# Kernel tuning notes

Measured on AMD Instinct MI355X. Metric: run time of the kernel, lower is better.

Reference implementation:

```python
import jax, jax.numpy as jnp
import numpy as np

H = 16          # num_heads
K = 15          # kernel_size (padding_l = K-1, causal)
EPS = 1e-5      # LayerNorm eps


def setup_inputs() -> dict:
    key = jax.random.key(0)
    ks = jax.random.split(key, 8)
    T, B, C, F = 1024, 8, 1024, 4096
    n = lambda k, shape, scale=1.0: jax.random.normal(k, shape, jnp.float32) * scale
    return {
        "x": n(ks[0], (T, B, C)),
        "w_lin": n(ks[1], (C, H * K), 0.02),      # dynamic-conv weight projection
        "b_lin": jnp.zeros((H * K,), jnp.float32),
        "ln_g": jnp.ones((C,), jnp.float32),
        "ln_b": jnp.zeros((C,), jnp.float32),
        "fc1_w": n(ks[2], (C, F), 0.02),
        "fc1_b": jnp.zeros((F,), jnp.float32),
        "fc2_w": n(ks[3], (F, C), 0.02),
        "fc2_b": jnp.zeros((C,), jnp.float32),
    }


def _dynamic_conv(x, w_lin, b_lin):
    # x: (T, B, C). Per-timestep weights -> softmax over kernel -> causal conv.
    T, B, C = x.shape
    R = C // H  # channels per head
    w = jnp.einsum('tbc,ck->tbk', x, w_lin) + b_lin          # (T, B, H*K)
    w = jax.nn.softmax(w.reshape(T, B, H, K), axis=-1)        # softmax over kernel taps
    # causal left-padding: tap k sees x[t + k - (K-1)]
    xp = jnp.pad(x, ((K - 1, 0), (0, 0), (0, 0))).reshape(T + K - 1, B, H, R)
    o = jnp.zeros((T, B, H, R), x.dtype)
    for k in range(K):  # fixed small kernel loop; avoids (T,B,C,K) unfold tensor
        o = o + w[:, :, :, k:k + 1] * xp[k:k + T]
    return o.reshape(T, B, C)


def _layer_norm(y, g, b):
    mu = jnp.mean(y, axis=-1, keepdims=True)
    var = jnp.var(y, axis=-1, keepdims=True)
    return (y - mu) * jax.lax.rsqrt(var + EPS) * g + b


def _forward(x, w_lin, b_lin, ln_g, ln_b, fc1_w, fc1_b, fc2_w, fc2_b):
    y = _dynamic_conv(x, w_lin, b_lin)
    y = _layer_norm(y, ln_g, ln_b)
    h = jax.nn.relu(jnp.einsum('tbc,cf->tbf', y, fc1_w) + fc1_b)
    out = jnp.einsum('tbf,fc->tbc', h, fc2_w) + fc2_b
    return out + y  # residual around FFN (residual taken post-LayerNorm)


def reference(x, w_lin, b_lin, ln_g, ln_b, fc1_w, fc1_b, fc2_w, fc2_b):
    return _forward(x, w_lin, b_lin, ln_g, ln_b, fc1_w, fc1_b, fc2_w, fc2_b)
```

## Files before the change

kernel.cpp:

```cpp
#include <hip/hip_runtime.h>


#define T_DIM 1024
#define B_DIM 8
#define C_DIM 1024
#define F_DIM 4096
#define H_DIM 16
#define K_TAP 15
#define TB (T_DIM * B_DIM)

typedef __attribute__((ext_vector_type(8))) short short8;
typedef __attribute__((ext_vector_type(4))) float f32x4;

__device__ __forceinline__ float bf2f(unsigned short u) {
    union { unsigned int i; float f; } v; v.i = ((unsigned int)u) << 16; return v.f;
}
__device__ __forceinline__ unsigned short f2bf(float f) {
    union { float f; unsigned int i; } v; v.f = f;
    unsigned int r = v.i + 0x7fffu + ((v.i >> 16) & 1u);
    return (unsigned short)(r >> 16);
}

__device__ __forceinline__ void async_copy16(const void* gptr, void* lptr) {
    __builtin_amdgcn_global_load_lds(
        (const __attribute__((address_space(1))) void*)gptr,
        (__attribute__((address_space(3))) void*)lptr, 16, 0, 0);
}

__global__ __launch_bounds__(256)
void prep(const float* __restrict__ x, unsigned short* __restrict__ xb,
          const float* __restrict__ fc1_w, unsigned short* __restrict__ fc1T,
          const float* __restrict__ fc2_w, unsigned short* __restrict__ fc2T,
          const float* __restrict__ w_lin, unsigned short* __restrict__ wlinT) {
    const int bid = blockIdx.x;
    const int tid = threadIdx.x;
    if (bid < 2048) {
        const int idx = bid * 256 + tid;
#pragma unroll
        for (int it = 0; it < 4; it++) {
            int i = (idx + it * 524288) * 4;
            float4 v = *(const float4*)(x + i);
            uint2 o;
            o.x = (unsigned int)f2bf(v.x) | ((unsigned int)f2bf(v.y) << 16);
            o.y = (unsigned int)f2bf(v.z) | ((unsigned int)f2bf(v.w) << 16);
            *(uint2*)(xb + i) = o;
        }
        return;
    }
    const float* in; unsigned short* out; int R, Cin, c0, r0;
    if (bid < 3072) {
        int idx = bid - 2048;
        in = fc1_w; out = fc1T; R = C_DIM; Cin = F_DIM;
        c0 = (idx & 63) * 64; r0 = (idx >> 6) * 64;
    } else if (bid < 4096) {
        int idx = bid - 3072;
        in = fc2_w; out = fc2T; R = F_DIM; Cin = C_DIM;
        c0 = (idx & 15) * 64; r0 = (idx >> 4) * 64;
    } else {
        int idx = bid - 4096;
        in = w_lin; out = wlinT; R = C_DIM; Cin = 240;
        c0 = (idx & 3) * 64; r0 = (idx >> 2) * 64;
    }
    __shared__ unsigned short tile[64][65];
    const int xx = tid & 63, yy = tid >> 6;
#pragma unroll
    for (int j = 0; j < 16; j++) {
        int r = r0 + yy + j * 4, c = c0 + xx;
        unsigned short v = 0;
        if (c < Cin) v = f2bf(in[(size_t)r * Cin + c]);
        tile[yy + j * 4][xx] = v;
    }
    __syncthreads();
#pragma unroll
    for (int j = 0; j < 16; j++) {
        out[(size_t)(c0 + yy + j * 4) * R + (r0 + xx)] = tile[xx][yy + j * 4];
    }
}

template <int MODE, int SWAP>
__global__ __launch_bounds__(256)
void gemm_bt(const unsigned short* __restrict__ A,
             const unsigned short* __restrict__ Bt,
             void* __restrict__ Cout_v,
             int M, int N, int K, int kz,
             const float* __restrict__ bias,
             const unsigned short* __restrict__ resid) {
    __shared__ __align__(16) unsigned short As[2][128 * 64];
    __shared__ __align__(16) unsigned short Bs[2][128 * 64];

    const int tid = threadIdx.x;
    const int m0 = (SWAP ? blockIdx.x : blockIdx.y) * 128;
    const int n0 = (SWAP ? blockIdx.y : blockIdx.x) * 128;
    const int kbase = blockIdx.z * kz;
    const int wave = tid >> 6, lane = tid & 63;
    const int quad = lane >> 4, l16 = lane & 15;
    const int wm = (wave >> 1) * 64;
    const int wn = (wave & 1) * 64;

    f32x4 acc[4][4];
#pragma unroll
    for (int i = 0; i < 4; i++)
#pragma unroll
        for (int j = 0; j < 4; j++) acc[i][j] = (f32x4){0.f, 0.f, 0.f, 0.f};

    const int rsub = lane >> 3;
    const int gch = (lane & 7) ^ rsub;
    const unsigned short* gA = A + (size_t)(m0 + wave * 32 + rsub) * K + kbase + gch * 8;
    const unsigned short* gB = Bt + (size_t)(n0 + wave * 32 + rsub) * K + kbase + gch * 8;
    unsigned short* lA[2] = {&As[0][wave * 32 * 64], &As[1][wave * 32 * 64]};
    unsigned short* lB[2] = {&Bs[0][wave * 32 * 64], &Bs[1][wave * 32 * 64]};

#pragma unroll
    for (int j = 0; j < 4; j++) {
        async_copy16(gA + (size_t)j * 8 * K, lA[0] + j * 8 * 64);
        async_copy16(gB + (size_t)j * 8 * K, lB[0] + j * 8 * 64);
    }

    const int swz = l16 & 7;
    int buf = 0;
    for (int k0 = 0; k0 < kz; k0 += 64) {
        __syncthreads();

        const int nk = k0 + 64;
        if (nk < kz) {
            const int nb = buf ^ 1;
#pragma unroll
            for (int j = 0; j < 4; j++) {
                async_copy16(gA + nk + (size_t)j * 8 * K, lA[nb] + j * 8 * 64);
                async_copy16(gB + nk + (size_t)j * 8 * K, lB[nb] + j * 8 * 64);
            }
        }

        short8 af[2][4], bfr[2][4];
#pragma unroll
        for (int kk = 0; kk < 2; kk++) {
            const int c = kk * 4 + quad;
#pragma unroll
            for (int i = 0; i < 4; i++) {
                af[kk][i]  = *(const short8*)(&As[buf][(wm + i * 16 + l16) * 64 + (c ^ swz) * 8]);
                bfr[kk][i] = *(const short8*)(&Bs[buf][(wn + i * 16 + l16) * 64 + (c ^ swz) * 8]);
            }
        }
#pragma unroll
        for (int kk = 0; kk < 2; kk++)
#pragma unroll
            for (int mi = 0; mi < 4; mi++)
#pragma unroll
                for (int nj = 0; nj < 4; nj++)
                    acc[mi][nj] = __builtin_amdgcn_mfma_f32_16x16x32_bf16(
                        af[kk][mi], bfr[kk][nj], acc[mi][nj], 0, 0, 0);
        buf ^= 1;
    }

    const int crow0 = m0 + wm + quad * 4;
    const int ccol0 = n0 + wn + l16;
    if (MODE == 3) {
        float* Cf = (float*)Cout_v + (size_t)blockIdx.z * M * N;
#pragma unroll
        for (int mi = 0; mi < 4; mi++)
#pragma unroll
            for (int i = 0; i < 4; i++) {
                int rr = crow0 + mi * 16 + i;
#pragma unroll
                for (int nj = 0; nj < 4; nj++)
                    Cf[(size_t)rr * N + ccol0 + nj * 16] = acc[mi][nj][i];
            }
    } else if (MODE == 1) {
        unsigned short* Cb = (unsigned short*)Cout_v;
        float bv[4];
#pragma unroll
        for (int nj = 0; nj < 4; nj++) bv[nj] = bias[ccol0 + nj * 16];
#pragma unroll
        for (int mi = 0; mi < 4; mi++)
#pragma unroll
            for (int i = 0; i < 4; i++) {
                int rr = crow0 + mi * 16 + i;
#pragma unroll
                for (int nj = 0; nj < 4; nj++) {
                    float v = fmaxf(acc[mi][nj][i] + bv[nj], 0.f);
                    Cb[(size_t)rr * N + ccol0 + nj * 16] = f2bf(v);
                }
            }
    } else {
        float* Cf = (float*)Cout_v;
        float bv[4];
#pragma unroll
        for (int nj = 0; nj < 4; nj++) bv[nj] = bias[ccol0 + nj * 16];
#pragma unroll
        for (int mi = 0; mi < 4; mi++)
#pragma unroll
            for (int i = 0; i < 4; i++) {
                int rr = crow0 + mi * 16 + i;
#pragma unroll
                for (int nj = 0; nj < 4; nj++) {
                    float v = acc[mi][nj][i] + bv[nj]
                            + bf2f(resid[(size_t)rr * N + ccol0 + nj * 16]);
                    Cf[(size_t)rr * N + ccol0 + nj * 16] = v;
                }
            }
    }
}

#define XSP 1032
#define WS_STRIDE ((size_t)TB * 256)
__global__ __launch_bounds__(256)
void conv_ln16s(const unsigned short* __restrict__ xb,
                const float* __restrict__ wscore,
                const float* __restrict__ b_lin,
                const float* __restrict__ ln_g,
                const float* __restrict__ ln_b,
                unsigned short* __restrict__ y) {
    __shared__ __align__(16) unsigned short xs[30 * XSP];
    __shared__ float wls[16 * 240];
    const int blk = blockIdx.x;
    const int b = blk & 7;
    const int t0 = (blk >> 3) * 16;
    const int tid = threadIdx.x;
    const int wave = tid >> 6, lane = tid & 63;

    for (int s = wave; s < 60; s += 4) {
        const int row = s >> 1, half = s & 1;
        const int t = t0 + row - 14;
        unsigned short* ldst = &xs[row * XSP + half * 512];
        if (t >= 0) {
            const unsigned short* src =
                xb + ((size_t)t * B_DIM + b) * C_DIM + half * 512 + lane * 8;
            async_copy16(src, ldst);
        } else {
            *(uint4*)(ldst + lane * 8) = make_uint4(0u, 0u, 0u, 0u);
        }
    }

    {
        const int row = tid >> 4, hh = tid & 15;
        const size_t grow = (size_t)(t0 + row) * B_DIM + b;
        const float* p = wscore + grow * 256 + hh * K_TAP;
        float v[K_TAP], mx = -1e30f;
#pragma unroll
        for (int k = 0; k < K_TAP; k++) {
            v[k] = p[k] + p[k + WS_STRIDE] + b_lin[hh * K_TAP + k];
            mx = fmaxf(mx, v[k]);
        }
        float s = 0.f;
#pragma unroll
        for (int k = 0; k < K_TAP; k++) { v[k] = __expf(v[k] - mx); s += v[k]; }
        float inv = 1.0f / s;
#pragma unroll
        for (int k = 0; k < K_TAP; k++) wls[row * 240 + hh * K_TAP + k] = v[k] * inv;
    }
    __syncthreads();

    const int chA = lane * 8;
    const int chB = 512 + lane * 8;
    const int hA = lane >> 3;
    const int hB = 8 + (lane >> 3);
    for (int rj = wave; rj < 16; rj += 4) {
        float o[16];
#pragma unroll
        for (int i = 0; i < 16; i++) o[i] = 0.f;
#pragma unroll
        for (int k = 0; k < K_TAP; k++) {
            float wA = wls[rj * 240 + hA * K_TAP + k];
            float wB = wls[rj * 240 + hB * K_TAP + k];
            const unsigned short* xr = &xs[(rj + k) * XSP];
            uint4 pA = *(const uint4*)(xr + chA);
            uint4 pB = *(const uint4*)(xr + chB);
            unsigned int ua[4] = {pA.x, pA.y, pA.z, pA.w};
            unsigned int ub[4] = {pB.x, pB.y, pB.z, pB.w};
#pragma unroll
            for (int q = 0; q < 4; q++) {
                o[2 * q]     += wA * bf2f((unsigned short)(ua[q] & 0xffff));
                o[2 * q + 1] += wA * bf2f((unsigned short)(ua[q] >> 16));
                o[8 + 2 * q]     += wB * bf2f((unsigned short)(ub[q] & 0xffff));
                o[8 + 2 * q + 1] += wB * bf2f((unsigned short)(ub[q] >> 16));
            }
        }
        float s = 0.f, s2 = 0.f;
#pragma unroll
        for (int i = 0; i < 16; i++) { s += o[i]; s2 += o[i] * o[i]; }
#pragma unroll
        for (int off = 32; off > 0; off >>= 1) {
            s  += __shfl_xor(s, off, 64);
            s2 += __shfl_xor(s2, off, 64);
        }
        float mu = s * (1.0f / C_DIM);
        float var = s2 * (1.0f / C_DIM) - mu * mu;
        float rs = rsqrtf(var + 1e-5f);

        unsigned short o16[16];
#pragma unroll
        for (int i = 0; i < 8; i++)
            o16[i] = f2bf((o[i] - mu) * rs * ln_g[chA + i] + ln_b[chA + i]);
#pragma unroll
        for (int i = 0; i < 8; i++)
            o16[8 + i] = f2bf((o[8 + i] - mu) * rs * ln_g[chB + i] + ln_b[chB + i]);
        uint4 w0, w1;
        w0.x = (unsigned int)o16[0]  | ((unsigned int)o16[1]  << 16);
        w0.y = (unsigned int)o16[2]  | ((unsigned int)o16[3]  << 16);
        w0.z = (unsigned int)o16[4]  | ((unsigned int)o16[5]  << 16);
        w0.w = (unsigned int)o16[6]  | ((unsigned int)o16[7]  << 16);
        w1.x = (unsigned int)o16[8]  | ((unsigned int)o16[9]  << 16);
        w1.y = (unsigned int)o16[10] | ((unsigned int)o16[11] << 16);
        w1.z = (unsigned int)o16[12] | ((unsigned int)o16[13] << 16);
        w1.w = (unsigned int)o16[14] | ((unsigned int)o16[15] << 16);
        unsigned short* yr = y + ((size_t)(t0 + rj) * B_DIM + b) * C_DIM;
        *(uint4*)(yr + chA) = w0;
        *(uint4*)(yr + chB) = w1;
    }
}

extern "C" void kernel_launch(void* const* d_in, const int* in_sizes, int n_in,
                              void* d_out, int out_size, void* d_ws, size_t ws_size,
                              hipStream_t stream) {
    const float* x     = (const float*)d_in[0];
    const float* w_lin = (const float*)d_in[1];
    const float* b_lin = (const float*)d_in[2];
    const float* ln_g  = (const float*)d_in[3];
    const float* ln_b  = (const float*)d_in[4];
    const float* fc1_w = (const float*)d_in[5];
    const float* fc1_b = (const float*)d_in[6];
    const float* fc2_w = (const float*)d_in[7];
    const float* fc2_b = (const float*)d_in[8];
    float* out = (float*)d_out;

    char* ws = (char*)d_ws;
    unsigned short* xb    = (unsigned short*)(ws);
    unsigned short* fc1T  = (unsigned short*)(ws + 16777216);
    unsigned short* fc2T  = (unsigned short*)(ws + 25165824);
    unsigned short* wlinT = (unsigned short*)(ws + 33554432);
    unsigned short* y     = (unsigned short*)(ws + 34078720);
    unsigned short* h     = (unsigned short*)(ws + 50855936);
    float* wscore = (float*)(ws + 50855936);

    prep<<<4160, 256, 0, stream>>>(x, xb, fc1_w, fc1T, fc2_w, fc2T, w_lin, wlinT);

    gemm_bt<3, 0><<<dim3(256 / 128, TB / 128, 2), 256, 0, stream>>>(
        xb, wlinT, (void*)wscore, TB, 256, C_DIM, C_DIM / 2, nullptr, nullptr);

    conv_ln16s<<<TB / 16, 256, 0, stream>>>(xb, wscore, b_lin, ln_g, ln_b, y);

    gemm_bt<1, 0><<<dim3(F_DIM / 128, TB / 128, 1), 256, 0, stream>>>(
        y, fc1T, (void*)h, TB, F_DIM, C_DIM, C_DIM, fc1_b, nullptr);

    gemm_bt<2, 1><<<dim3(TB / 128, C_DIM / 128, 1), 256, 0, stream>>>(
        h, fc2T, (void*)out, TB, C_DIM, F_DIM, F_DIM, fc2_b, y);
}
```

Measured before the change: 298.7 us.

## Fuse x bf16 conversion and weight-projection GEMM into conv+LayerNorm kernel

Drops the separate fp32→bf16 conversion of x and the split-K weight-score GEMM. The conv kernel now loads fp32 x directly, converts it into shared memory, and computes the 16×240 per-block softmax logits with MFMA against wlinT. This removes the global round trips for xb and wscore and two launches. In exchange, each conv block recomputes the projection with a small, poorly-utilized MFMA loop that reads wlinT from global memory, and x rows are re-read across the overlapping time windows.

```diff
diff --git a/kernel.cpp b/kernel.cpp
--- a/kernel.cpp
+++ b/kernel.cpp
@@ -28,36 +28,22 @@
 }
 
 __global__ __launch_bounds__(256)
-void prep(const float* __restrict__ x, unsigned short* __restrict__ xb,
-          const float* __restrict__ fc1_w, unsigned short* __restrict__ fc1T,
+void prep(const float* __restrict__ fc1_w, unsigned short* __restrict__ fc1T,
           const float* __restrict__ fc2_w, unsigned short* __restrict__ fc2T,
           const float* __restrict__ w_lin, unsigned short* __restrict__ wlinT) {
     const int bid = blockIdx.x;
     const int tid = threadIdx.x;
-    if (bid < 2048) {
-        const int idx = bid * 256 + tid;
-#pragma unroll
-        for (int it = 0; it < 4; it++) {
-            int i = (idx + it * 524288) * 4;
-            float4 v = *(const float4*)(x + i);
-            uint2 o;
-            o.x = (unsigned int)f2bf(v.x) | ((unsigned int)f2bf(v.y) << 16);
-            o.y = (unsigned int)f2bf(v.z) | ((unsigned int)f2bf(v.w) << 16);
-            *(uint2*)(xb + i) = o;
-        }
-        return;
-    }
     const float* in; unsigned short* out; int R, Cin, c0, r0;
-    if (bid < 3072) {
-        int idx = bid - 2048;
+    if (bid < 1024) {
+        int idx = bid;
         in = fc1_w; out = fc1T; R = C_DIM; Cin = F_DIM;
         c0 = (idx & 63) * 64; r0 = (idx >> 6) * 64;
-    } else if (bid < 4096) {
-        int idx = bid - 3072;
+    } else if (bid < 2048) {
+        int idx = bid - 1024;
         in = fc2_w; out = fc2T; R = F_DIM; Cin = C_DIM;
         c0 = (idx & 15) * 64; r0 = (idx >> 4) * 64;
     } else {
-        int idx = bid - 4096;
+        int idx = bid - 2048;
         in = w_lin; out = wlinT; R = C_DIM; Cin = 240;
         c0 = (idx & 3) * 64; r0 = (idx >> 2) * 64;
     }
@@ -154,18 +140,7 @@
 
     const int crow0 = m0 + wm + quad * 4;
     const int ccol0 = n0 + wn + l16;
-    if (MODE == 3) {
-        float* Cf = (float*)Cout_v + (size_t)blockIdx.z * M * N;
-#pragma unroll
-        for (int mi = 0; mi < 4; mi++)
-#pragma unroll
-            for (int i = 0; i < 4; i++) {
-                int rr = crow0 + mi * 16 + i;
-#pragma unroll
-                for (int nj = 0; nj < 4; nj++)
-                    Cf[(size_t)rr * N + ccol0 + nj * 16] = acc[mi][nj][i];
-            }
-    } else if (MODE == 1) {
+    if (MODE == 1) {
         unsigned short* Cb = (unsigned short*)Cout_v;
         float bv[4];
 #pragma unroll
@@ -202,14 +177,13 @@
 }
 
 #define XSP 1032
-#define WS_STRIDE ((size_t)TB * 256)
 __global__ __launch_bounds__(256)
-void conv_ln16s(const unsigned short* __restrict__ xb,
-                const float* __restrict__ wscore,
-                const float* __restrict__ b_lin,
-                const float* __restrict__ ln_g,
-                const float* __restrict__ ln_b,
-                unsigned short* __restrict__ y) {
+void megaconv(const float* __restrict__ x,
+              const unsigned short* __restrict__ wlinT,
+              const float* __restrict__ b_lin,
+              const float* __restrict__ ln_g,
+              const float* __restrict__ ln_b,
+              unsigned short* __restrict__ y) {
     __shared__ __align__(16) unsigned short xs[30 * XSP];
     __shared__ float wls[16 * 240];
     const int blk = blockIdx.x;
@@ -217,28 +191,57 @@
     const int t0 = (blk >> 3) * 16;
     const int tid = threadIdx.x;
     const int wave = tid >> 6, lane = tid & 63;
-
-    for (int s = wave; s < 60; s += 4) {
-        const int row = s >> 1, half = s & 1;
-        const int t = t0 + row - 14;
-        unsigned short* ldst = &xs[row * XSP + half * 512];
+    const int quad = lane >> 4, l16 = lane & 15;
+
+#pragma unroll
+    for (int j = 0; j < 30; j++) {
+        const int t = t0 + j - 14;
+        uint2 o = make_uint2(0u, 0u);
         if (t >= 0) {
-            const unsigned short* src =
-                xb + ((size_t)t * B_DIM + b) * C_DIM + half * 512 + lane * 8;
-            async_copy16(src, ldst);
-        } else {
-            *(uint4*)(ldst + lane * 8) = make_uint4(0u, 0u, 0u, 0u);
-        }
-    }
+            float4 v = *(const float4*)(x + ((size_t)t * B_DIM + b) * C_DIM + tid * 4);
+            o.x = (unsigned int)f2bf(v.x) | ((unsigned int)f2bf(v.y) << 16);
+            o.y = (unsigned int)f2bf(v.z) | ((unsigned int)f2bf(v.w) << 16);
+        }
+        *(uint2*)(&xs[j * XSP + tid * 4]) = o;
+    }
+    __syncthreads();
+
+    {
+        f32x4 lacc[4];
+#pragma unroll
+        for (int i = 0; i < 4; i++) lacc[i] = (f32x4){0.f, 0.f, 0.f, 0.f};
+        const unsigned short* xrow = &xs[(14 + l16) * XSP + quad * 8];
+        const unsigned short* brow = wlinT + (size_t)l16 * C_DIM + quad * 8;
+#pragma unroll 8
+        for (int kk = 0; kk < 32; kk++) {
+            short8 af = *(const short8*)(xrow + kk * 32);
+#pragma unroll
+            for (int j = 0; j < 4; j++) {
+                const int nt = wave + j * 4;
+                if (nt < 15) {
+                    short8 bf = *(const short8*)(brow + (size_t)nt * 16 * C_DIM + kk * 32);
+                    lacc[j] = __builtin_amdgcn_mfma_f32_16x16x32_bf16(af, bf, lacc[j], 0, 0, 0);
+                }
+            }
+        }
+#pragma unroll
+        for (int j = 0; j < 4; j++) {
+            const int nt = wave + j * 4;
+            if (nt < 15) {
+#pragma unroll
+                for (int i = 0; i < 4; i++)
+                    wls[(quad * 4 + i) * 240 + nt * 16 + l16] = lacc[j][i];
+            }
+        }
+    }
+    __syncthreads();
 
     {
         const int row = tid >> 4, hh = tid & 15;
-        const size_t grow = (size_t)(t0 + row) * B_DIM + b;
-        const float* p = wscore + grow * 256 + hh * K_TAP;
         float v[K_TAP], mx = -1e30f;
 #pragma unroll
         for (int k = 0; k < K_TAP; k++) {
-            v[k] = p[k] + p[k + WS_STRIDE] + b_lin[hh * K_TAP + k];
+            v[k] = wls[row * 240 + hh * K_TAP + k] + b_lin[hh * K_TAP + k];
             mx = fmaxf(mx, v[k]);
         }
         float s = 0.f;
@@ -324,20 +327,15 @@
     float* out = (float*)d_out;
 
     char* ws = (char*)d_ws;
-    unsigned short* xb    = (unsigned short*)(ws);
     unsigned short* fc1T  = (unsigned short*)(ws + 16777216);
     unsigned short* fc2T  = (unsigned short*)(ws + 25165824);
     unsigned short* wlinT = (unsigned short*)(ws + 33554432);
     unsigned short* y     = (unsigned short*)(ws + 34078720);
     unsigned short* h     = (unsigned short*)(ws + 50855936);
-    float* wscore = (float*)(ws + 50855936);
-
-    prep<<<4160, 256, 0, stream>>>(x, xb, fc1_w, fc1T, fc2_w, fc2T, w_lin, wlinT);
-
-    gemm_bt<3, 0><<<dim3(256 / 128, TB / 128, 2), 256, 0, stream>>>(
-        xb, wlinT, (void*)wscore, TB, 256, C_DIM, C_DIM / 2, nullptr, nullptr);
-
-    conv_ln16s<<<TB / 16, 256, 0, stream>>>(xb, wscore, b_lin, ln_g, ln_b, y);
+
+    prep<<<2112, 256, 0, stream>>>(fc1_w, fc1T, fc2_w, fc2T, w_lin, wlinT);
+
+    megaconv<<<TB / 16, 256, 0, stream>>>(x, wlinT, b_lin, ln_g, ln_b, y);
 
     gemm_bt<1, 0><<<dim3(F_DIM / 128, TB / 128, 1), 256, 0, stream>>>(
         y, fc1T, (void*)h, TB, F_DIM, C_DIM, C_DIM, fc1_b, nullptr);
```

New measurement: 359.0 us. 1.2x slower.
